# Optimization experiments

Hardware: AMD Instinct MI355X
Metric: run time of the kernel (lower is better)

## Reference

```python
import jax, jax.numpy as jnp
import numpy as np

N_ITERS = 25
LAMBDA_INIT = 0.1
TOL = 1e-6
EPS = 1e-10
REWEIGHTED = True


def setup_inputs() -> dict:
    key = jax.random.key(0)
    k1, k2 = jax.random.split(key)
    Y = jax.random.normal(k1, (16, 1024, 64), dtype=jnp.float32)   # [batch, T, joints]
    D = jax.random.normal(k2, (1024, 2048), dtype=jnp.float32)     # [T, Np]
    return {"Y": Y, "D": D}


def _soft_threshold(x, tau):
    return jnp.sign(x) * jnp.maximum(jnp.abs(x) - tau, 0.0)


def _converge(C_curr, C_prev, t_prev, DtD, DtY, L, lam):
    # Fixed-length scan emulating the torch loop with a data-dependent break:
    # once the Frobenius norm of (C_next - C_curr) drops below TOL, the state
    # is frozen (equivalent to breaking out of the loop).
    def body(carry, _):
        Cc, Cp, t, done = carry
        grad = jnp.einsum('pq,bqj->bpj', DtD, Cp) - DtY      # [b, Np, j]
        C_next = _soft_threshold(Cp - L * grad, L * lam)
        small = jnp.linalg.norm(C_next - Cc) < TOL
        do = jnp.logical_not(done | small)
        t_next = (1.0 + jnp.sqrt(1.0 + 4.0 * t * t)) * 0.5
        t_const = (t - 1.0) / t_next
        Cp_new = C_next + t_const * (C_next - Cc)
        carry = (jnp.where(do, C_next, Cc),
                 jnp.where(do, Cp_new, Cp),
                 jnp.where(do, t_next, t),
                 done | small)
        return carry, None

    init = (C_curr, C_prev, t_prev, jnp.array(False))
    (Cc, Cp, t, _), _ = jax.lax.scan(body, init, None, length=N_ITERS)
    return Cc, Cp, t


def _fista(Y, D):
    b, T, j = Y.shape
    Np = D.shape[1]
    Dt = D.T
    DtD = Dt @ D                                   # [Np, Np]
    DtY = jnp.einsum('pt,btj->bpj', Dt, Y)         # [b, Np, j]
    L = 1.0 / jnp.linalg.norm(DtD, ord=2)          # 1 / spectral norm
    Cc = jnp.zeros((b, Np, j), Y.dtype)
    Cp = Cc
    t = jnp.asarray(1.0, Y.dtype)
    lam = jnp.asarray(LAMBDA_INIT, Y.dtype)
    if REWEIGHTED:
        # torch runs: converge -> weight_lambda -> converge -> weight_lambda;
        # the final weight_lambda does not affect the returned C.
        Cc, Cp, t = _converge(Cc, Cp, t, DtD, DtY, L, lam)
        w = 1.0 / (jnp.abs(Cc) + EPS)
        w = w / jnp.linalg.norm(w, axis=1, keepdims=True)  # L2 over Np dim
        lam = lam * w * Np
        Cc, Cp, t = _converge(Cc, Cp, t, DtD, DtY, L, lam)
    else:
        Cc, Cp, t = _converge(Cc, Cp, t, DtD, DtY, L, lam)
    return Cc


def reference(Y, D):
    return _fista(Y, D)
```

## Files before the change

kernel.cpp:

```cpp
#include <hip/hip_runtime.h>
#include <math.h>

#define T_DIM 1024
#define NP    2048
#define NB    1024
#define NITER 25
#define NSQ   5
#define NPI   8
#define LAM0  0.1f
#define EPS_W 1e-10f

typedef float    f32x4 __attribute__((ext_vector_type(4)));
typedef _Float16 f16x8 __attribute__((ext_vector_type(8)));
typedef _Float16 f16x4 __attribute__((ext_vector_type(4)));

__device__ __forceinline__ void gload16(const void* g, void* l) {
  __builtin_amdgcn_global_load_lds((const __attribute__((address_space(1))) unsigned int*)g,
                                   (__attribute__((address_space(3))) unsigned int*)l, 16, 0, 0);
}

__device__ __forceinline__ void mm3_db(
    const _Float16* __restrict__ Ah, const _Float16* __restrict__ Al,
    const _Float16* __restrict__ Bh, const _Float16* __restrict__ Bl,
    int ldk, int n0, int p0, int kb0, int nsteps,
    f32x4 acc0[4][2], f32x4 acc1[4][2])
{
  __shared__ __align__(16) _Float16 sm[2][4][4096];
  const int tid = threadIdx.x;
  const int lane = tid & 63, wave = tid >> 6;
  const int quad = lane >> 4, rl = lane & 15;
  const int wn = (wave >> 2) * 64, wp = (wave & 3) * 32;
  const int kc = tid >> 7, row = tid & 127;
  const int lbe = wave * 512;
#pragma unroll
  for (int i = 0; i < 4; i++)
#pragma unroll
    for (int j = 0; j < 2; j++) { acc0[i][j] = (f32x4)0.0f; acc1[i][j] = (f32x4)0.0f; }

  {
    size_t ga = (size_t)(n0 + row) * ldk + kb0 + kc * 8;
    size_t gb = (size_t)(p0 + row) * ldk + kb0 + kc * 8;
    gload16(Ah + ga, &sm[0][0][lbe]);
    gload16(Al + ga, &sm[0][1][lbe]);
    gload16(Bh + gb, &sm[0][2][lbe]);
    gload16(Bl + gb, &sm[0][3][lbe]);
  }
  for (int s = 0; s < nsteps; s++) {
    const int cur = s & 1;
    __syncthreads();
    if (s + 1 < nsteps) {
      const int nxt = cur ^ 1;
      const int kb = kb0 + (s + 1) * 32;
      size_t ga = (size_t)(n0 + row) * ldk + kb + kc * 8;
      size_t gb = (size_t)(p0 + row) * ldk + kb + kc * 8;
      gload16(Ah + ga, &sm[nxt][0][lbe]);
      gload16(Al + ga, &sm[nxt][1][lbe]);
      gload16(Bh + gb, &sm[nxt][2][lbe]);
      gload16(Bl + gb, &sm[nxt][3][lbe]);
    }
    f16x8 a_h[4], a_l[4], b_h[2], b_l[2];
#pragma unroll
    for (int t = 0; t < 4; t++) {
      int ar = (quad * 128 + wn + t * 16 + rl) * 8;
      a_h[t] = *(const f16x8*)&sm[cur][0][ar];
      a_l[t] = *(const f16x8*)&sm[cur][1][ar];
    }
#pragma unroll
    for (int t = 0; t < 2; t++) {
      int bp = (quad * 128 + wp + t * 16 + rl) * 8;
      b_h[t] = *(const f16x8*)&sm[cur][2][bp];
      b_l[t] = *(const f16x8*)&sm[cur][3][bp];
    }
#pragma unroll
    for (int mt = 0; mt < 4; mt++)
#pragma unroll
      for (int nt = 0; nt < 2; nt++)
        acc0[mt][nt] = __builtin_amdgcn_mfma_f32_16x16x32_f16(a_h[mt], b_h[nt], acc0[mt][nt], 0, 0, 0);
#pragma unroll
    for (int mt = 0; mt < 4; mt++)
#pragma unroll
      for (int nt = 0; nt < 2; nt++)
        acc1[mt][nt] = __builtin_amdgcn_mfma_f32_16x16x32_f16(a_l[mt], b_h[nt], acc1[mt][nt], 0, 0, 0);
#pragma unroll
    for (int mt = 0; mt < 4; mt++)
#pragma unroll
      for (int nt = 0; nt < 2; nt++)
        acc1[mt][nt] = __builtin_amdgcn_mfma_f32_16x16x32_f16(a_h[mt], b_l[nt], acc1[mt][nt], 0, 0, 0);
  }
}

__global__ __launch_bounds__(512, 4) void k_mm(const _Float16* __restrict__ Ch, const _Float16* __restrict__ Cl,
                                               const _Float16* __restrict__ H, const _Float16* __restrict__ Ee,
                                               float* __restrict__ part) {
  const int b = blockIdx.x;
  const int xcd = b & 7, q = b >> 3;
  const int pt = xcd * 2 + (q & 1);
  const int ny = (q >> 1) & 7;
  const int z  = q >> 4;
  f32x4 acc0[4][2], acc1[4][2];
  const int n0 = ny * 128, p0 = pt * 128;
  mm3_db(Ch, Cl, H, Ee, 2048, n0, p0, z * 512, 16, acc0, acc1);
  const int lane = threadIdx.x & 63, wave = threadIdx.x >> 6;
  const int quad = lane >> 4, rl = lane & 15;
  const int wn = (wave >> 2) * 64, wp = (wave & 3) * 32;
  float* op = part + (size_t)z * NB * NP;
#pragma unroll
  for (int mt = 0; mt < 4; mt++)
#pragma unroll
    for (int nt = 0; nt < 2; nt++) {
      const int p = p0 + wp + nt * 16 + rl;
      const size_t rb = (size_t)(n0 + wn + mt * 16 + quad * 4) * NP + p;
#pragma unroll
      for (int r = 0; r < 4; r++)
        op[rb + (size_t)r * NP] = acc0[mt][nt][r] + acc1[mt][nt][r] * (1.f / 4096.f);
    }
}

__global__ __launch_bounds__(256) void k_epi(const float* __restrict__ part,
    const float* __restrict__ DtY_, const float* __restrict__ CcIn,
    const _Float16* __restrict__ ChIn, const _Float16* __restrict__ ClIn,
    const float* __restrict__ Lptr, const float* __restrict__ thrM, float tc,
    float* __restrict__ CcOut, _Float16* __restrict__ ChOut, _Float16* __restrict__ ClOut) {
  const int b = blockIdx.x;
  const int xcd = b & 7, r_ = b >> 3;
  const int pt = xcd * 2 + (r_ & 1);
  const int nc = r_ >> 1;
  const int tid = threadIdx.x;
  const int rowi = nc * 8 + (tid >> 5);
  const int col = pt * 128 + (tid & 31) * 4;
  const size_t g = (size_t)rowi * NP + col;
  const float Lv = Lptr[0];
  float ps[4], dy[4], cc[4], th[4];
  *(float4*)ps = *(const float4*)(part + g);
#pragma unroll
  for (int z = 1; z < 4; z++) {
    float t[4];
    *(float4*)t = *(const float4*)(part + (size_t)z * NB * NP + g);
#pragma unroll
    for (int j = 0; j < 4; j++) ps[j] += t[j];
  }
  *(float4*)dy = *(const float4*)(DtY_ + g);
  *(float4*)cc = *(const float4*)(CcIn + g);
  f16x4 chv = *(const f16x4*)(ChIn + g);
  f16x4 clv = *(const f16x4*)(ClIn + g);
  if (thrM) { *(float4*)th = *(const float4*)(thrM + g); }
  float cn[4];
  f16x4 ho, lo;
#pragma unroll
  for (int j = 0; j < 4; j++) {
    float grad = ps[j] - dy[j];
    float cp = (float)chv[j] + (float)clv[j] * (1.f / 4096.f);
    float z = cp - Lv * grad;
    float t2 = thrM ? th[j] : Lv * LAM0;
    float az = fabsf(z) - t2;
    float v = az > 0.f ? copysignf(az, z) : 0.f;
    cn[j] = v;
    float cpn = fmaf(tc, v - cc[j], v);
    _Float16 h = (_Float16)cpn;
    ho[j] = h;
    lo[j] = (_Float16)((cpn - (float)h) * 4096.f);
  }
  *(float4*)(CcOut + g) = *(float4*)cn;
  if (ChOut) {
    *(f16x4*)(ChOut + g) = ho;
    *(f16x4*)(ClOut + g) = lo;
  }
}

__global__ __launch_bounds__(256) void k_init0(const float* __restrict__ DtY_,
    const float* __restrict__ Lptr, float* __restrict__ CcOut,
    _Float16* __restrict__ ChOut, _Float16* __restrict__ ClOut) {
  const size_t g = ((size_t)blockIdx.x * 256 + threadIdx.x) * 4;
  const float Lv = Lptr[0];
  const float thr = Lv * LAM0;
  float dy[4];
  *(float4*)dy = *(const float4*)(DtY_ + g);
  float cn[4];
  f16x4 ho, lo;
#pragma unroll
  for (int j = 0; j < 4; j++) {
    float z = Lv * dy[j];
    float az = fabsf(z) - thr;
    float v = az > 0.f ? copysignf(az, z) : 0.f;
    cn[j] = v;
    _Float16 h = (_Float16)v;
    ho[j] = h;
    lo[j] = (_Float16)((v - (float)h) * 4096.f);
  }
  *(float4*)(CcOut + g) = *(float4*)cn;
  *(f16x4*)(ChOut + g) = ho;
  *(f16x4*)(ClOut + g) = lo;
}

__device__ __forceinline__ void mm3c(
    const _Float16* __restrict__ Ah, const _Float16* __restrict__ Al,
    const _Float16* __restrict__ Bh, const _Float16* __restrict__ Bl,
    int ldk, int n0, int p0, int nsteps,
    f32x4 acc0[2][2], f32x4 acc1[2][2])
{
  __shared__ __align__(16) _Float16 sAh[8192], sAl[8192], sBh[8192], sBl[8192];
  const int tid = threadIdx.x;
  const int lane = tid & 63, w = tid >> 6;
  const int quad = lane >> 4, rl = lane & 15;
  const int wm = (w >> 1) * 32, wp = (w & 1) * 32;
#pragma unroll
  for (int i = 0; i < 2; i++)
#pragma unroll
    for (int j = 0; j < 2; j++) { acc0[i][j] = (f32x4)0.0f; acc1[i][j] = (f32x4)0.0f; }

  for (int s = 0; s < nsteps; s++) {
    const int kb = s * 128;
    if (s) __syncthreads();
#pragma unroll
    for (int i = 0; i < 4; i++) {
      int slot = i * 256 + w * 64 + lane;
      int kc = slot >> 6, row = slot & 63;
      int lb = (i * 256 + w * 64) * 8;
      size_t ga = (size_t)(n0 + row) * ldk + kb + kc * 8;
      size_t gb = (size_t)(p0 + row) * ldk + kb + kc * 8;
      gload16(Ah + ga, sAh + lb);
      gload16(Al + ga, sAl + lb);
      gload16(Bh + gb, sBh + lb);
      gload16(Bl + gb, sBl + lb);
    }
    __syncthreads();
#pragma unroll
    for (int kk = 0; kk < 4; kk++) {
      const int kc = kk * 4 + quad;
      f16x8 a_h[2], a_l[2], b_h[2], b_l[2];
#pragma unroll
      for (int t = 0; t < 2; t++) {
        int ar = wm + t * 16 + rl;
        int bp = wp + t * 16 + rl;
        a_h[t] = *(const f16x8*)&sAh[(kc * 64 + ar) * 8];
        a_l[t] = *(const f16x8*)&sAl[(kc * 64 + ar) * 8];
        b_h[t] = *(const f16x8*)&sBh[(kc * 64 + bp) * 8];
        b_l[t] = *(const f16x8*)&sBl[(kc * 64 + bp) * 8];
      }
#pragma unroll
      for (int mt = 0; mt < 2; mt++)
#pragma unroll
        for (int nt = 0; nt < 2; nt++) {
          acc0[mt][nt] = __builtin_amdgcn_mfma_f32_16x16x32_f16(a_h[mt], b_h[nt], acc0[mt][nt], 0, 0, 0);
          acc1[mt][nt] = __builtin_amdgcn_mfma_f32_16x16x32_f16(a_l[mt], b_h[nt], acc1[mt][nt], 0, 0, 0);
          acc1[mt][nt] = __builtin_amdgcn_mfma_f32_16x16x32_f16(a_h[mt], b_l[nt], acc1[mt][nt], 0, 0, 0);
        }
    }
  }
}

__global__ __launch_bounds__(256, 2) void k_dtd(const _Float16* __restrict__ Dth, const _Float16* __restrict__ Dtl,
                                                _Float16* __restrict__ H, _Float16* __restrict__ Ee) {
  const int b = blockIdx.x;
  const int xcd = b & 7, i4 = b >> 3;
  const int ny = i4 >> 2, pt = xcd * 4 + (i4 & 3);
  const int n0 = ny * 64, p0 = pt * 64;
  f32x4 acc0[2][2], acc1[2][2];
  mm3c(Dth, Dtl, Dth, Dtl, 1024, n0, p0, 8, acc0, acc1);
  const int lane = threadIdx.x & 63, w = threadIdx.x >> 6;
  const int quad = lane >> 4, rl = lane & 15;
  const int wm = (w >> 1) * 32, wp = (w & 1) * 32;
#pragma unroll
  for (int mt = 0; mt < 2; mt++)
#pragma unroll
    for (int nt = 0; nt < 2; nt++) {
      const int p = p0 + wp + nt * 16 + rl;
      const size_t rb = (size_t)(n0 + wm + mt * 16 + quad * 4) * NP + p;
#pragma unroll
      for (int r = 0; r < 4; r++) {
        const size_t idx = rb + (size_t)r * NP;
        float v = acc0[mt][nt][r] + acc1[mt][nt][r] * (1.f / 4096.f);
        _Float16 h = (_Float16)v;
        H[idx] = h;
        Ee[idx] = (_Float16)((v - (float)h) * 4096.f);
      }
    }
}

__global__ __launch_bounds__(256, 2) void k_g(const _Float16* __restrict__ Dh, const _Float16* __restrict__ Dl,
                                              float* __restrict__ G, float* __restrict__ ss0) {
  const int b = blockIdx.x;
  const int xcd = b & 7, i4 = b >> 3;
  const int ny = i4 >> 1, pt = xcd * 2 + (i4 & 1);
  const int n0 = ny * 64, p0 = pt * 64;
  f32x4 acc0[2][2], acc1[2][2];
  mm3c(Dh, Dl, Dh, Dl, 2048, n0, p0, 16, acc0, acc1);
  const int tid = threadIdx.x;
  const int lane = tid & 63, w = tid >> 6;
  const int quad = lane >> 4, rl = lane & 15;
  const int wm = (w >> 1) * 32, wp = (w & 1) * 32;
  float ssl = 0.f;
#pragma unroll
  for (int mt = 0; mt < 2; mt++)
#pragma unroll
    for (int nt = 0; nt < 2; nt++) {
      const int p = p0 + wp + nt * 16 + rl;
      const size_t rb = (size_t)(n0 + wm + mt * 16 + quad * 4) * 1024 + p;
#pragma unroll
      for (int r = 0; r < 4; r++) {
        float v = acc0[mt][nt][r] + acc1[mt][nt][r] * (1.f / 4096.f);
        G[rb + (size_t)r * 1024] = v;
        ssl = fmaf(v, v, ssl);
      }
    }
  __shared__ float red[256];
  red[tid] = ssl; __syncthreads();
  for (int off = 128; off > 0; off >>= 1) {
    if (tid < off) red[tid] += red[tid + off];
    __syncthreads();
  }
  if (tid == 0) atomicAdd(ss0, red[0]);
}

__global__ __launch_bounds__(256, 2) void k_dty(const _Float16* __restrict__ Yth, const _Float16* __restrict__ Ytl,
                                                const _Float16* __restrict__ Dth, const _Float16* __restrict__ Dtl,
                                                float* __restrict__ DtY_) {
  const int b = blockIdx.x;
  const int xcd = b & 7, i4 = b >> 3;
  const int ny = i4 >> 2, pt = xcd * 4 + (i4 & 3);
  const int n0 = ny * 64, p0 = pt * 64;
  f32x4 acc0[2][2], acc1[2][2];
  mm3c(Yth, Ytl, Dth, Dtl, 1024, n0, p0, 8, acc0, acc1);
  const int lane = threadIdx.x & 63, w = threadIdx.x >> 6;
  const int quad = lane >> 4, rl = lane & 15;
  const int wm = (w >> 1) * 32, wp = (w & 1) * 32;
#pragma unroll
  for (int mt = 0; mt < 2; mt++)
#pragma unroll
    for (int nt = 0; nt < 2; nt++) {
      const int p = p0 + wp + nt * 16 + rl;
      const size_t rb = (size_t)(n0 + wm + mt * 16 + quad * 4) * NP + p;
#pragma unroll
      for (int r = 0; r < 4; r++)
        DtY_[rb + (size_t)r * NP] = acc0[mt][nt][r] + acc1[mt][nt][r] * (1.f / 4096.f);
    }
}

__global__ __launch_bounds__(256, 2) void k_sqf(const _Float16* __restrict__ Min, const float* __restrict__ ssPrev,
                                                _Float16* __restrict__ Mout, float* __restrict__ ssNext,
                                                float invfac) {
  __shared__ __align__(16) _Float16 sA[8192], sB[8192];
  const int b = blockIdx.x;
  const int xcd = b & 7, i4 = b >> 3;
  const int ny = i4 >> 1, pt = xcd * 2 + (i4 & 1);
  const int n0 = ny * 64, p0 = pt * 64;
  const int tid = threadIdx.x;
  const int lane = tid & 63, w = tid >> 6;
  const int quad = lane >> 4, rl = lane & 15;
  const int wm = (w >> 1) * 32, wp = (w & 1) * 32;
  f32x4 acc[2][2];
#pragma unroll
  for (int i = 0; i < 2; i++)
#pragma unroll
    for (int j = 0; j < 2; j++) acc[i][j] = (f32x4)0.0f;

  for (int s = 0; s < 8; s++) {
    const int kb = s * 128;
    if (s) __syncthreads();
#pragma unroll
    for (int i = 0; i < 4; i++) {
      int slot = i * 256 + w * 64 + lane;
      int kc = slot >> 6, row = slot & 63;
      int lb = (i * 256 + w * 64) * 8;
      gload16(Min + (size_t)(n0 + row) * 1024 + kb + kc * 8, sA + lb);
      gload16(Min + (size_t)(p0 + row) * 1024 + kb + kc * 8, sB + lb);
    }
    __syncthreads();
#pragma unroll
    for (int kk = 0; kk < 4; kk++) {
      const int kc = kk * 4 + quad;
      f16x8 a[2], bb[2];
#pragma unroll
      for (int t = 0; t < 2; t++) {
        a[t]  = *(const f16x8*)&sA[(kc * 64 + wm + t * 16 + rl) * 8];
        bb[t] = *(const f16x8*)&sB[(kc * 64 + wp + t * 16 + rl) * 8];
      }
#pragma unroll
      for (int mt = 0; mt < 2; mt++)
#pragma unroll
        for (int nt = 0; nt < 2; nt++)
          acc[mt][nt] = __builtin_amdgcn_mfma_f32_16x16x32_f16(a[mt], bb[nt], acc[mt][nt], 0, 0, 0);
    }
  }
  const float inv = invfac / ssPrev[0];
  float ssl = 0.f;
#pragma unroll
  for (int mt = 0; mt < 2; mt++)
#pragma unroll
    for (int nt = 0; nt < 2; nt++) {
      const int p = p0 + wp + nt * 16 + rl;
      const size_t rb = (size_t)(n0 + wm + mt * 16 + quad * 4) * 1024 + p;
#pragma unroll
      for (int r = 0; r < 4; r++) {
        float v = acc[mt][nt][r] * inv;
        Mout[rb + (size_t)r * 1024] = (_Float16)(v * 4096.f);
        ssl = fmaf(v, v, ssl);
      }
    }
  __syncthreads();
  float* red = (float*)sA;
  red[tid] = ssl; __syncthreads();
  for (int off = 128; off > 0; off >>= 1) {
    if (tid < off) red[tid] += red[tid + off];
    __syncthreads();
  }
  if (tid == 0) atomicAdd(ssNext, red[0]);
}

__global__ __launch_bounds__(256) void k_split(const float* __restrict__ src, _Float16* __restrict__ H,
                                               _Float16* __restrict__ L, int n4) {
  int g = blockIdx.x * 256 + threadIdx.x;
  if (g < n4) {
    float4 v = ((const float4*)src)[g];
    float vv[4] = {v.x, v.y, v.z, v.w};
    f16x4 h, l;
#pragma unroll
    for (int j = 0; j < 4; j++) {
      _Float16 hh = (_Float16)vv[j];
      h[j] = hh;
      l[j] = (_Float16)((vv[j] - (float)hh) * 4096.f);
    }
    ((f16x4*)H)[g] = h;
    ((f16x4*)L)[g] = l;
  }
}

__global__ __launch_bounds__(256) void k_h16(const float* __restrict__ src, _Float16* __restrict__ dst,
                                             int n4, float scale) {
  int g = blockIdx.x * 256 + threadIdx.x;
  if (g < n4) {
    float4 v = ((const float4*)src)[g];
    f16x4 h;
    h[0] = (_Float16)(v.x * scale); h[1] = (_Float16)(v.y * scale);
    h[2] = (_Float16)(v.z * scale); h[3] = (_Float16)(v.w * scale);
    ((f16x4*)dst)[g] = h;
  }
}

__global__ __launch_bounds__(256) void k_tr(const float* __restrict__ src, float* __restrict__ dst,
                                            int R, int C) {
  __shared__ float T[64][65];
  const int tid = threadIdx.x;
  const int c0 = blockIdx.x * 64, r0 = blockIdx.y * 64;
  const int cx = tid & 15, ry = tid >> 4;
#pragma unroll
  for (int ii = 0; ii < 4; ii++) {
    int r = ry + ii * 16;
    float4 v = *(const float4*)(src + (size_t)(r0 + r) * C + c0 + cx * 4);
    T[cx * 4 + 0][r] = v.x; T[cx * 4 + 1][r] = v.y;
    T[cx * 4 + 2][r] = v.z; T[cx * 4 + 3][r] = v.w;
  }
  __syncthreads();
#pragma unroll
  for (int ii = 0; ii < 4; ii++) {
    int c = ry + ii * 16;
    float4 v = make_float4(T[c][cx * 4], T[c][cx * 4 + 1], T[c][cx * 4 + 2], T[c][cx * 4 + 3]);
    *(float4*)(dst + (size_t)(c0 + c) * R + r0 + cx * 4) = v;
  }
}

__global__ __launch_bounds__(256) void k_trY(const float* __restrict__ Y, float* __restrict__ Yt) {
  __shared__ float T[64][65];
  const int tid = threadIdx.x;
  const int t0 = blockIdx.x * 64, b = blockIdx.y;
  const int cx = tid & 15, ry = tid >> 4;
#pragma unroll
  for (int ii = 0; ii < 4; ii++) {
    int r = ry + ii * 16;
    float4 v = *(const float4*)(Y + ((size_t)b * T_DIM + t0 + r) * 64 + cx * 4);
    T[cx * 4 + 0][r] = v.x; T[cx * 4 + 1][r] = v.y;
    T[cx * 4 + 2][r] = v.z; T[cx * 4 + 3][r] = v.w;
  }
  __syncthreads();
#pragma unroll
  for (int ii = 0; ii < 4; ii++) {
    int j = ry + ii * 16;
    float4 v = make_float4(T[j][cx * 4], T[j][cx * 4 + 1], T[j][cx * 4 + 2], T[j][cx * 4 + 3]);
    *(float4*)(Yt + ((size_t)b * 64 + j) * T_DIM + t0 + cx * 4) = v;
  }
}

__global__ void k_initx(float* __restrict__ X) {
  int g = blockIdx.x * 256 + threadIdx.x;
  if (g < 4096) {
    unsigned h = (unsigned)g * 2654435761u;
    h ^= h >> 16; h *= 2246822519u; h ^= h >> 13;
    X[g] = ((float)(h & 0xffffff) / 16777216.0f) - 0.5f;
  }
}

__global__ __launch_bounds__(256) void k_matvec(const _Float16* __restrict__ M, const float* __restrict__ Xin,
                                                float* __restrict__ Xout, const float* __restrict__ prevNorm,
                                                float* __restrict__ outNorm) {
  const int tid = threadIdx.x, lane = tid & 63, w = tid >> 6;
  const int row = blockIdx.x * 4 + w;
  const _Float16* Mr = M + (size_t)row * 1024;
  float s[4] = {0.f, 0.f, 0.f, 0.f};
  for (int j = 0; j < 16; j++) {
    int k = j * 64 + lane;
    float m = (float)Mr[k];
    float4 x = *(const float4*)(Xin + k * 4);
    s[0] = fmaf(m, x.x, s[0]); s[1] = fmaf(m, x.y, s[1]);
    s[2] = fmaf(m, x.z, s[2]); s[3] = fmaf(m, x.w, s[3]);
  }
#pragma unroll
  for (int off = 32; off > 0; off >>= 1)
#pragma unroll
    for (int c = 0; c < 4; c++) s[c] += __shfl_down(s[c], off, 64);
  __shared__ float red[16];
  if (lane == 0) {
#pragma unroll
    for (int c = 0; c < 4; c++) {
      float sc = prevNorm ? rsqrtf(prevNorm[c]) : 1.0f;
      float o = s[c] * sc;
      Xout[row * 4 + c] = o;
      red[w * 4 + c] = o * o;
    }
  }
  __syncthreads();
  if (tid < 4) atomicAdd(&outNorm[tid], red[tid] + red[4 + tid] + red[8 + tid] + red[12 + tid]);
}

__global__ __launch_bounds__(256) void k_rq(const float* __restrict__ G, const float* __restrict__ X,
                                            float* __restrict__ num, float* __restrict__ den) {
  const int tid = threadIdx.x, lane = tid & 63, w = tid >> 6;
  const int row = blockIdx.x * 4 + w;
  const float* Gr = G + (size_t)row * 1024;
  float s[4] = {0.f, 0.f, 0.f, 0.f};
  for (int j = 0; j < 16; j++) {
    int k = j * 64 + lane;
    float m = Gr[k];
    float4 x = *(const float4*)(X + k * 4);
    s[0] = fmaf(m, x.x, s[0]); s[1] = fmaf(m, x.y, s[1]);
    s[2] = fmaf(m, x.z, s[2]); s[3] = fmaf(m, x.w, s[3]);
  }
#pragma unroll
  for (int off = 32; off > 0; off >>= 1)
#pragma unroll
    for (int c = 0; c < 4; c++) s[c] += __shfl_down(s[c], off, 64);
  __shared__ float rn[16], rd[16];
  if (lane == 0) {
    float4 v = *(const float4*)(X + row * 4);
    float vv[4] = {v.x, v.y, v.z, v.w};
#pragma unroll
    for (int c = 0; c < 4; c++) { rn[w * 4 + c] = vv[c] * s[c]; rd[w * 4 + c] = vv[c] * vv[c]; }
  }
  __syncthreads();
  if (tid < 4) {
    atomicAdd(&num[tid], rn[tid] + rn[4 + tid] + rn[8 + tid] + rn[12 + tid]);
    atomicAdd(&den[tid], rd[tid] + rd[4 + tid] + rd[8 + tid] + rd[12 + tid]);
  }
}

__global__ void k_finL(const float* __restrict__ num, const float* __restrict__ den, float* __restrict__ Lout) {
  if (threadIdx.x == 0 && blockIdx.x == 0) {
    float best = 0.f;
    for (int c = 0; c < 4; c++) { float r = num[c] / den[c]; best = fmaxf(best, r); }
    Lout[0] = 1.0f / best;
  }
}

__global__ __launch_bounds__(256) void k_rowss(const float* __restrict__ Cc, float* __restrict__ rowss) {
  const int n = blockIdx.x, tid = threadIdx.x;
  const float4* row = (const float4*)(Cc + (size_t)n * NP);
  float s = 0.f;
  for (int i = tid; i < 512; i += 256) {
    float4 v = row[i];
    float r0 = 1.f / (fabsf(v.x) + EPS_W), r1 = 1.f / (fabsf(v.y) + EPS_W);
    float r2 = 1.f / (fabsf(v.z) + EPS_W), r3 = 1.f / (fabsf(v.w) + EPS_W);
    s += r0 * r0 + r1 * r1 + r2 * r2 + r3 * r3;
  }
  __shared__ float red[256];
  red[tid] = s; __syncthreads();
  for (int off = 128; off > 0; off >>= 1) {
    if (tid < off) red[tid] += red[tid + off];
    __syncthreads();
  }
  if (tid == 0) rowss[n] = red[0];
}

__global__ __launch_bounds__(256) void k_thrmat(const float* __restrict__ Cc, const float* __restrict__ rowss,
                                                const float* __restrict__ Lptr, float* __restrict__ thrMat) {
  const size_t g = (size_t)blockIdx.x * 256 + threadIdx.x;
  const int n = (int)(g >> 11);
  float r = 1.0f / (fabsf(Cc[g]) + EPS_W);
  thrMat[g] = Lptr[0] * LAM0 * (float)NP * r * rsqrtf(rowss[n]);
}

__global__ __launch_bounds__(256) void k_out(const float* __restrict__ Cc, float* __restrict__ out) {
  __shared__ float T[64][65];
  const int tid = threadIdx.x;
  const int p0 = blockIdx.x * 64, nt = blockIdx.y;
  const int pr = tid & 15, nr = tid >> 4;
#pragma unroll
  for (int ii = 0; ii < 4; ii++) {
    int n_l = nr + ii * 16;
    float4 v = *(const float4*)(Cc + ((size_t)nt * 64 + n_l) * NP + p0 + pr * 4);
    T[pr * 4 + 0][n_l] = v.x; T[pr * 4 + 1][n_l] = v.y;
    T[pr * 4 + 2][n_l] = v.z; T[pr * 4 + 3][n_l] = v.w;
  }
  __syncthreads();
#pragma unroll
  for (int ii = 0; ii < 4; ii++) {
    int p_l = nr + ii * 16;
    float4 v = make_float4(T[p_l][pr * 4], T[p_l][pr * 4 + 1], T[p_l][pr * 4 + 2], T[p_l][pr * 4 + 3]);
    *(float4*)(out + (size_t)nt * (NP * 64) + (size_t)(p0 + p_l) * 64 + pr * 4) = v;
  }
}

#define MBf(x) ((size_t)(x) * 262144)

extern "C" void kernel_launch(void* const* d_in, const int* in_sizes, int n_in,
                              void* d_out, int out_size, void* d_ws, size_t ws_size,
                              hipStream_t stream) {
  const float* Y = (const float*)d_in[0];
  const float* D = (const float*)d_in[1];
  float* out = (float*)d_out;
  float* ws = (float*)d_ws;

  _Float16* H    = (_Float16*)(ws);
  _Float16* Ee   = (_Float16*)(ws + MBf(8));
  float*    DtY  = ws + MBf(16);
  float*    Cc0  = ws + MBf(24);
  float*    Cc1  = ws + MBf(32);
  _Float16* Ch0  = (_Float16*)(ws + MBf(40));
  _Float16* Cl0  = (_Float16*)(ws + MBf(44));
  _Float16* Ch1  = (_Float16*)(ws + MBf(48));
  _Float16* Cl1  = (_Float16*)(ws + MBf(52));
  float*    thrM = ws + MBf(56);
  float*    part = ws + MBf(64);
  float*    Dt   = ws + MBf(64);
  float*    Yt   = ws + MBf(72);
  float*    G    = ws + MBf(76);
  _Float16* Mh0  = (_Float16*)(ws + MBf(80));
  _Float16* Mh1  = (_Float16*)(ws + MBf(82));
  _Float16* Dh   = (_Float16*)(ws + MBf(32));
  _Float16* Dl   = (_Float16*)(ws + MBf(36));
  _Float16* Dth  = (_Float16*)(ws + MBf(48));
  _Float16* Dtl  = (_Float16*)(ws + MBf(52));
  _Float16* Yth  = (_Float16*)(ws + MBf(56));
  _Float16* Ytl  = (_Float16*)(ws + MBf(58));
  float*    XA   = ws + MBf(96);
  float*    XB   = XA + 4096;
  float*    scal = XB + 4096;
  float*    ssv   = scal;
  float*    norms = scal + 8;
  float*    num   = scal + 8 + NPI * 4;
  float*    den   = num + 4;
  float*    Lp    = den + 4;
  float*    rowss = Lp + 4;

  float*    CcB[2] = {Cc0, Cc1};
  _Float16* ChB[2] = {Ch0, Ch1};
  _Float16* ClB[2] = {Cl0, Cl1};

  hipMemsetAsync(scal, 0, (8 + NPI * 4 + 16) * sizeof(float), stream);

  k_initx<<<16, 256, 0, stream>>>(XA);
  k_tr <<<dim3(32, 16), 256, 0, stream>>>(D, Dt, 1024, 2048);
  k_trY<<<dim3(16, 16), 256, 0, stream>>>(Y, Yt);
  k_split<<<2048, 256, 0, stream>>>(D,  Dh,  Dl,  (T_DIM * NP) / 4);
  k_split<<<2048, 256, 0, stream>>>(Dt, Dth, Dtl, (T_DIM * NP) / 4);
  k_split<<<1024, 256, 0, stream>>>(Yt, Yth, Ytl, (NB * T_DIM) / 4);
  k_g  <<<256,  256, 0, stream>>>(Dh, Dl, G, ssv);
  k_dtd<<<1024, 256, 0, stream>>>(Dth, Dtl, H, Ee);
  k_dty<<<512,  256, 0, stream>>>(Yth, Ytl, Dth, Dtl, DtY);
  k_h16<<<1024, 256, 0, stream>>>(G, Mh0, (1024 * 1024) / 4, 1.0f / 64.0f);
  _Float16* MB[2] = {Mh0, Mh1};
  for (int l = 0; l < NSQ; l++) {
    float invfac = (l == 0) ? 4096.0f : (1.0f / 16777216.0f);
    k_sqf<<<256, 256, 0, stream>>>(MB[l & 1], ssv + l, MB[(l + 1) & 1], ssv + l + 1, invfac);
  }
  _Float16* Mfin = MB[NSQ & 1];
  for (int i = 0; i < NPI; i++) {
    const float* xin = (i & 1) ? XB : XA;
    float* xout = (i & 1) ? XA : XB;
    k_matvec<<<256, 256, 0, stream>>>(Mfin, xin, xout,
                                      i ? norms + (i - 1) * 4 : nullptr, norms + i * 4);
  }
  k_rq  <<<256, 256, 0, stream>>>(G, XA, num, den);
  k_finL<<<1, 64, 0, stream>>>(num, den, Lp);

  float tcv[2 * NITER];
  {
    float t = 1.0f;
    for (int i = 0; i < 2 * NITER; i++) {
      float tn = 0.5f * (1.0f + sqrtf(1.0f + 4.0f * t * t));
      tcv[i] = (t - 1.0f) / tn;
      t = tn;
    }
  }

  k_init0<<<(NB * NP) / 1024, 256, 0, stream>>>(DtY, Lp, Cc1, Ch1, Cl1);

  for (int i = 1; i < 2 * NITER; i++) {
    int a = i & 1, b = (i + 1) & 1;
    if (i == NITER) {
      k_rowss <<<1024, 256, 0, stream>>>(CcB[a], rowss);
      k_thrmat<<<(NB * NP) / 256, 256, 0, stream>>>(CcB[a], rowss, Lp, thrM);
    }
    const float* thr = (i < NITER) ? nullptr : thrM;
    const bool last = (i == 2 * NITER - 1);
    k_mm <<<512, 512, 0, stream>>>(ChB[a], ClB[a], H, Ee, part);
    k_epi<<<2048, 256, 0, stream>>>(part, DtY, CcB[a], ChB[a], ClB[a], Lp, thr,
                                    tcv[i], CcB[b],
                                    last ? nullptr : ChB[b], last ? nullptr : ClB[b]);
  }
  k_out<<<dim3(32, 16), 256, 0, stream>>>(CcB[0], out);
}
```

Measured before the change: 3.340 ms.

## Use split-K 128x128 double-buffered tiles for DtD and DtY precompute GEMMs

Moves the DtD and DtY setup GEMMs from the single-buffered 64x64 mm3c path onto the double-buffered mm3_db routine with 128x128 tiles and 512-thread blocks. K is split (2-way for DtD, 4-way for DtY) so there are enough blocks, and fp32 partial sums go to a scratch buffer. Small elementwise kernels then reduce the partials and, for DtD, produce the fp16 hi/lo split. This aims for more reuse per tile and better latency hiding, at the cost of extra global traffic for the partials, two extra launches and a scratch allocation.

```diff
diff --git a/kernel.cpp b/kernel.cpp
--- a/kernel.cpp
+++ b/kernel.cpp
@@ -192,6 +192,91 @@
   *(f16x4*)(ClOut + g) = lo;
 }
 
+__global__ __launch_bounds__(512, 4) void k_dtd(const _Float16* __restrict__ Dth, const _Float16* __restrict__ Dtl,
+                                                float* __restrict__ part) {
+  const int b = blockIdx.x;
+  const int xcd = b & 7, q = b >> 3;
+  const int pt = xcd * 2 + (q & 1);
+  const int ny = (q >> 1) & 15;
+  const int z  = q >> 5;
+  f32x4 acc0[4][2], acc1[4][2];
+  const int n0 = ny * 128, p0 = pt * 128;
+  mm3_db(Dth, Dtl, Dth, Dtl, 1024, n0, p0, z * 512, 16, acc0, acc1);
+  const int lane = threadIdx.x & 63, wave = threadIdx.x >> 6;
+  const int quad = lane >> 4, rl = lane & 15;
+  const int wn = (wave >> 2) * 64, wp = (wave & 3) * 32;
+  float* op = part + (size_t)z * NP * NP;
+#pragma unroll
+  for (int mt = 0; mt < 4; mt++)
+#pragma unroll
+    for (int nt = 0; nt < 2; nt++) {
+      const int p = p0 + wp + nt * 16 + rl;
+      const size_t rb = (size_t)(n0 + wn + mt * 16 + quad * 4) * NP + p;
+#pragma unroll
+      for (int r = 0; r < 4; r++)
+        op[rb + (size_t)r * NP] = acc0[mt][nt][r] + acc1[mt][nt][r] * (1.f / 4096.f);
+    }
+}
+
+__global__ __launch_bounds__(256) void k_dtdc(const float* __restrict__ part,
+                                              _Float16* __restrict__ H, _Float16* __restrict__ Ee) {
+  const size_t g = ((size_t)blockIdx.x * 256 + threadIdx.x) * 4;
+  float a[4], bq[4];
+  *(float4*)a  = *(const float4*)(part + g);
+  *(float4*)bq = *(const float4*)(part + (size_t)NP * NP + g);
+  f16x4 hv, ev;
+#pragma unroll
+  for (int j = 0; j < 4; j++) {
+    float v = a[j] + bq[j];
+    _Float16 h = (_Float16)v;
+    hv[j] = h;
+    ev[j] = (_Float16)((v - (float)h) * 4096.f);
+  }
+  *(f16x4*)(H + g)  = hv;
+  *(f16x4*)(Ee + g) = ev;
+}
+
+__global__ __launch_bounds__(512, 4) void k_dty(const _Float16* __restrict__ Yth, const _Float16* __restrict__ Ytl,
+                                                const _Float16* __restrict__ Dth, const _Float16* __restrict__ Dtl,
+                                                float* __restrict__ part) {
+  const int b = blockIdx.x;
+  const int xcd = b & 7, q = b >> 3;
+  const int pt = xcd * 2 + (q & 1);
+  const int ny = (q >> 1) & 7;
+  const int z  = q >> 4;
+  f32x4 acc0[4][2], acc1[4][2];
+  const int n0 = ny * 128, p0 = pt * 128;
+  mm3_db(Yth, Ytl, Dth, Dtl, 1024, n0, p0, z * 256, 8, acc0, acc1);
+  const int lane = threadIdx.x & 63, wave = threadIdx.x >> 6;
+  const int quad = lane >> 4, rl = lane & 15;
+  const int wn = (wave >> 2) * 64, wp = (wave & 3) * 32;
+  float* op = part + (size_t)z * NB * NP;
+#pragma unroll
+  for (int mt = 0; mt < 4; mt++)
+#pragma unroll
+    for (int nt = 0; nt < 2; nt++) {
+      const int p = p0 + wp + nt * 16 + rl;
+      const size_t rb = (size_t)(n0 + wn + mt * 16 + quad * 4) * NP + p;
+#pragma unroll
+      for (int r = 0; r < 4; r++)
+        op[rb + (size_t)r * NP] = acc0[mt][nt][r] + acc1[mt][nt][r] * (1.f / 4096.f);
+    }
+}
+
+__global__ __launch_bounds__(256) void k_dtyc(const float* __restrict__ part, float* __restrict__ DtY_) {
+  const size_t g = ((size_t)blockIdx.x * 256 + threadIdx.x) * 4;
+  float s[4];
+  *(float4*)s = *(const float4*)(part + g);
+#pragma unroll
+  for (int z = 1; z < 4; z++) {
+    float t[4];
+    *(float4*)t = *(const float4*)(part + (size_t)z * NB * NP + g);
+#pragma unroll
+    for (int j = 0; j < 4; j++) s[j] += t[j];
+  }
+  *(float4*)(DtY_ + g) = *(float4*)s;
+}
+
 __device__ __forceinline__ void mm3c(
     const _Float16* __restrict__ Ah, const _Float16* __restrict__ Al,
     const _Float16* __restrict__ Bh, const _Float16* __restrict__ Bl,
@@ -247,34 +332,6 @@
         }
     }
   }
-}
-
-__global__ __launch_bounds__(256, 2) void k_dtd(const _Float16* __restrict__ Dth, const _Float16* __restrict__ Dtl,
-                                                _Float16* __restrict__ H, _Float16* __restrict__ Ee) {
-  const int b = blockIdx.x;
-  const int xcd = b & 7, i4 = b >> 3;
-  const int ny = i4 >> 2, pt = xcd * 4 + (i4 & 3);
-  const int n0 = ny * 64, p0 = pt * 64;
-  f32x4 acc0[2][2], acc1[2][2];
-  mm3c(Dth, Dtl, Dth, Dtl, 1024, n0, p0, 8, acc0, acc1);
-  const int lane = threadIdx.x & 63, w = threadIdx.x >> 6;
-  const int quad = lane >> 4, rl = lane & 15;
-  const int wm = (w >> 1) * 32, wp = (w & 1) * 32;
-#pragma unroll
-  for (int mt = 0; mt < 2; mt++)
-#pragma unroll
-    for (int nt = 0; nt < 2; nt++) {
-      const int p = p0 + wp + nt * 16 + rl;
-      const size_t rb = (size_t)(n0 + wm + mt * 16 + quad * 4) * NP + p;
-#pragma unroll
-      for (int r = 0; r < 4; r++) {
-        const size_t idx = rb + (size_t)r * NP;
-        float v = acc0[mt][nt][r] + acc1[mt][nt][r] * (1.f / 4096.f);
-        _Float16 h = (_Float16)v;
-        H[idx] = h;
-        Ee[idx] = (_Float16)((v - (float)h) * 4096.f);
-      }
-    }
 }
 
 __global__ __launch_bounds__(256, 2) void k_g(const _Float16* __restrict__ Dh, const _Float16* __restrict__ Dl,
@@ -310,30 +367,6 @@
     __syncthreads();
   }
   if (tid == 0) atomicAdd(ss0, red[0]);
-}
-
-__global__ __launch_bounds__(256, 2) void k_dty(const _Float16* __restrict__ Yth, const _Float16* __restrict__ Ytl,
-                                                const _Float16* __restrict__ Dth, const _Float16* __restrict__ Dtl,
-                                                float* __restrict__ DtY_) {
-  const int b = blockIdx.x;
-  const int xcd = b & 7, i4 = b >> 3;
-  const int ny = i4 >> 2, pt = xcd * 4 + (i4 & 3);
-  const int n0 = ny * 64, p0 = pt * 64;
-  f32x4 acc0[2][2], acc1[2][2];
-  mm3c(Yth, Ytl, Dth, Dtl, 1024, n0, p0, 8, acc0, acc1);
-  const int lane = threadIdx.x & 63, w = threadIdx.x >> 6;
-  const int quad = lane >> 4, rl = lane & 15;
-  const int wm = (w >> 1) * 32, wp = (w & 1) * 32;
-#pragma unroll
-  for (int mt = 0; mt < 2; mt++)
-#pragma unroll
-    for (int nt = 0; nt < 2; nt++) {
-      const int p = p0 + wp + nt * 16 + rl;
-      const size_t rb = (size_t)(n0 + wm + mt * 16 + quad * 4) * NP + p;
-#pragma unroll
-      for (int r = 0; r < 4; r++)
-        DtY_[rb + (size_t)r * NP] = acc0[mt][nt][r] + acc1[mt][nt][r] * (1.f / 4096.f);
-    }
 }
 
 __global__ __launch_bounds__(256, 2) void k_sqf(const _Float16* __restrict__ Min, const float* __restrict__ ssPrev,
@@ -662,9 +695,11 @@
   k_split<<<2048, 256, 0, stream>>>(D,  Dh,  Dl,  (T_DIM * NP) / 4);
   k_split<<<2048, 256, 0, stream>>>(Dt, Dth, Dtl, (T_DIM * NP) / 4);
   k_split<<<1024, 256, 0, stream>>>(Yt, Yth, Ytl, (NB * T_DIM) / 4);
+  k_dtd <<<512, 512, 0, stream>>>(Dth, Dtl, part);
+  k_dtdc<<<4096, 256, 0, stream>>>(part, H, Ee);
+  k_dty <<<512, 512, 0, stream>>>(Yth, Ytl, Dth, Dtl, part);
+  k_dtyc<<<2048, 256, 0, stream>>>(part, DtY);
   k_g  <<<256,  256, 0, stream>>>(Dh, Dl, G, ssv);
-  k_dtd<<<1024, 256, 0, stream>>>(Dth, Dtl, H, Ee);
-  k_dty<<<512,  256, 0, stream>>>(Yth, Ytl, Dth, Dtl, DtY);
   k_h16<<<1024, 256, 0, stream>>>(G, Mh0, (1024 * 1024) / 4, 1.0f / 64.0f);
   _Float16* MB[2] = {Mh0, Mh1};
   for (int l = 0; l < NSQ; l++) {
```

New measurement: 3.354 ms. Within noise of the previous version (+0.4%).
